# Optimization experiments

Measured on AMD Instinct MI355X. Metric: run time of the kernel, lower is better.

The kernel has to match this reference:

```python
import jax, jax.numpy as jnp
import numpy as np

TAU = 2.0          # spikingjelly LIFNode default
V_TH = 7.0         # from source
DECREASE = 0.5     # decrease_factor
ALPHA = 4.0        # sigmoid surrogate alpha (spikingjelly default)


@jax.custom_vjp
def spike(v):
    # Heaviside with sigmoid surrogate gradient
    return (v >= 0.0).astype(v.dtype)

def _spike_fwd(v):
    return spike(v), v

def _spike_bwd(v, g):
    s = jax.nn.sigmoid(ALPHA * v)
    return (g * ALPHA * s * (1.0 - s),)

spike.defvjp(_spike_fwd, _spike_bwd)


def setup_inputs() -> dict:
    key = jax.random.key(0)
    k1, k2, k3 = jax.random.split(key, 3)
    B, C, T = 4096, 14, 600
    x = jax.random.normal(k1, (B, C, T), dtype=jnp.float32)
    # weights: normal(mean=0.8, std=0.05) clamped to [0,1]; nn.Linear stores [out,in]
    W1 = jnp.clip(0.8 + 0.05 * jax.random.normal(k2, (14, 14), dtype=jnp.float32), 0.0, 1.0)
    W2 = jnp.clip(0.8 + 0.05 * jax.random.normal(k3, (500, 14), dtype=jnp.float32), 0.0, 1.0)
    return {"x": x, "W1": W1, "W2": W2}


def _forward(x, W1, W2):
    B = x.shape[0]
    xt = jnp.transpose(x, (2, 0, 1))  # [T, B, 14]

    v1_0 = jnp.zeros((B, 14), x.dtype)
    v2_0 = jnp.zeros((B, 500), x.dtype)
    cache0 = jnp.zeros((B, 14), x.dtype)

    def step(carry, x_t):
        v1, v2, cache = carry
        # block 1: linear + decayed feedback of previous spikes
        i1 = x_t @ W1.T + DECREASE * cache
        v1 = v1 + (i1 - v1) / TAU          # LIF charge (decay_input, v_reset=0)
        s1 = spike(v1 - V_TH)
        v1 = v1 * (1.0 - s1)               # hard reset to 0
        # block 2
        i2 = s1 @ W2.T
        v2 = v2 + (i2 - v2) / TAU
        s2 = spike(v2 - V_TH)
        v2 = v2 * (1.0 - s2)
        return (v1, v2, s1), None

    (v1, v2, cache), _ = jax.lax.scan(step, (v1_0, v2_0, cache0), xt)
    return jnp.exp(v2)  # liquid state [B, 500]


def reference(x, W1, W2):
    return _forward(x, W1, W2)
```

## Files before the change

### kernel.cpp

```cpp
#include <hip/hip_runtime.h>
#include <math.h>

#define T     600
#define C     14
#define NOUT  500
#define W     128
#define NWIN  5
#define DSTR  132
#define CAP   64

typedef float f32x2 __attribute__((ext_vector_type(2)));

__device__ __forceinline__ void stage16(const float* gp, float* lp) {
    __builtin_amdgcn_global_load_lds(
        (const __attribute__((address_space(1))) void*)(gp),
        (__attribute__((address_space(3))) void*)(lp), 16, 0, 0);
}

__global__ __launch_bounds__(64)
void snn_v8(const float* __restrict__ x, const float* __restrict__ W1,
            const float* __restrict__ W2, float* __restrict__ out) {
    __shared__ float    xs[448 * 4];
    __shared__ float    db[C * DSTR];
    __shared__ unsigned evs[CAP];

    const int  lane = threadIdx.x;
    const long row  = blockIdx.x;
    const float* xr = &x[row * (long)(C * T)];
    const int  ce   = (lane < C) ? lane : (C - 1);

    const float* gsrc[7];
    #pragma unroll
    for (int k = 0; k < 7; ++k) {
        const int s = 64 * k + lane;
        const int j = s >> 5;
        const int g = (s - j) & 31;
        gsrc[k] = xr + j * T + 4 * g;
    }
    int xadr[C];
    #pragma unroll
    for (int j = 0; j < C; ++j)
        xadr[j] = 16 * (32 * j + (((lane >> 1) + j) & 31)) + 8 * (lane & 1);

    #pragma unroll
    for (int k = 0; k < 7; ++k)
        stage16(gsrc[k], &xs[k * 256]);

    float v1 = 0.f;
    int   ecnt = 0;

    for (int w = 0; w < NWIN; ++w) {
        const int t0 = w * W;
        asm volatile("s_waitcnt vmcnt(0)" ::: "memory");
        __builtin_amdgcn_sched_barrier(0);

        f32x2 xv[C];
        #pragma unroll
        for (int j = 0; j < C; ++j)
            xv[j] = *(const f32x2*)((const char*)xs + xadr[j]);
        const float msk = (w == NWIN - 1 && 2 * lane >= T - 512) ? 0.f : 0.5f;
        #pragma unroll
        for (int j = 0; j < C; ++j) { xv[j].x *= msk; xv[j].y *= msk; }
        #pragma unroll
        for (int c = 0; c < C; ++c) {
            f32x2 a = {0.f, 0.f};
            #pragma unroll
            for (int j = 0; j < C; ++j) {
                const float wv = W1[c * C + j];
                a.x = fmaf(xv[j].x, wv, a.x);
                a.y = fmaf(xv[j].y, wv, a.y);
            }
            *(f32x2*)&db[c * DSTR + 2 * lane] = a;
        }
        asm volatile("s_waitcnt lgkmcnt(0)" ::: "memory");
        __builtin_amdgcn_sched_barrier(0);

        if (w + 1 < NWIN) {
            if (w + 1 < NWIN - 1) {
                #pragma unroll
                for (int k = 0; k < 7; ++k) {
                    gsrc[k] += W;
                    stage16(gsrc[k], &xs[k * 256]);
                }
            } else {
                #pragma unroll
                for (int k = 0; k < 7; ++k) {
                    gsrc[k] += W;
                    const int s = 64 * k + lane;
                    const int g = (s - (s >> 5)) & 31;
                    if (4 * g < T - 512)
                        stage16(gsrc[k], &xs[k * 256]);
                }
            }
        }

        const float* dp = &db[ce * DSTR];
        const int nb = (w < NWIN - 1) ? 8 : 6;
        float4 c0 = *(const float4*)&dp[0];
        float4 c1 = *(const float4*)&dp[4];
        float4 c2 = *(const float4*)&dp[8];
        float4 c3 = *(const float4*)&dp[12];
        for (int b = 0; b < nb; ++b) {
            float4 n0, n1, n2, n3;
            const bool more = (b + 1 < nb);
            if (more) {
                const float* np_ = dp + 16 * (b + 1);
                n0 = *(const float4*)&np_[0];
                n1 = *(const float4*)&np_[4];
                n2 = *(const float4*)&np_[8];
                n3 = *(const float4*)&np_[12];
            }
            float h[16];
            h[0]=c0.x; h[1]=c0.y; h[2]=c0.z; h[3]=c0.w;
            h[4]=c1.x; h[5]=c1.y; h[6]=c1.z; h[7]=c1.w;
            h[8]=c2.x; h[9]=c2.y; h[10]=c2.z; h[11]=c2.w;
            h[12]=c3.x; h[13]=c3.y; h[14]=c3.z; h[15]=c3.w;

            float vv = v1;
            float m0 = -1e30f, m1 = -1e30f, m2 = -1e30f, m3 = -1e30f;
            #pragma unroll
            for (int u = 0; u < 16; u += 4) {
                vv = fmaf(vv, 0.5f, h[u]);     m0 = fmaxf(m0, vv);
                vv = fmaf(vv, 0.5f, h[u + 1]); m1 = fmaxf(m1, vv);
                vv = fmaf(vv, 0.5f, h[u + 2]); m2 = fmaxf(m2, vv);
                vv = fmaf(vv, 0.5f, h[u + 3]); m3 = fmaxf(m3, vv);
            }
            const float mx = fmaxf(fmaxf(m0, m1), fmaxf(m2, m3));

            if (__builtin_expect(__ballot(mx >= 7.0f) != 0ull, 0)) {
                float vp = v1;
                #pragma unroll
                for (int u = 0; u < 16; ++u) {
                    vp = fmaf(vp, 0.5f, h[u]);
                    const unsigned long long bal = __ballot(vp >= 7.0f);
                    if (bal) {
                        if (vp >= 7.0f) vp = 0.5f;
                        if (lane == 0 && ecnt < CAP)
                            evs[ecnt] = ((unsigned)(t0 + 16 * b + u) << 14)
                                      | ((unsigned)bal & 0x3FFFu);
                        ++ecnt;
                    }
                }
                v1 = vp;
            } else {
                v1 = vv;
            }
            if (more) { c0 = n0; c1 = n1; c2 = n2; c3 = n3; }
        }
    }

    asm volatile("s_waitcnt lgkmcnt(0)" ::: "memory");
    __builtin_amdgcn_sched_barrier(0);

    const int n = (ecnt < CAP) ? ecnt : CAP;
    float v2[8];
    #pragma unroll
    for (int k = 0; k < 8; ++k) v2[k] = 0.f;
    int tprev = -1;

    for (int e = 0; e < n; ++e) {
        const unsigned ev = evs[e];
        const int t = (int)(ev >> 14);
        unsigned mm = ev & 0x3FFFu;
        float i2[8];
        #pragma unroll
        for (int k = 0; k < 8; ++k) i2[k] = 0.f;
        while (mm) {
            const int c = (int)__builtin_ctz(mm);
            mm &= mm - 1;
            #pragma unroll
            for (int k = 0; k < 8; ++k) {
                const int o = lane + (k << 6);
                if (o < NOUT) i2[k] += W2[o * C + c];
            }
        }
        const int gap = t - tprev - 1;
        if (gap > 0) {
            #pragma unroll
            for (int k = 0; k < 8; ++k) v2[k] = ldexpf(v2[k], -gap);
        }
        #pragma unroll
        for (int k = 0; k < 8; ++k) {
            const float v = v2[k] + (i2[k] - v2[k]) * 0.5f;
            v2[k] = (v >= 7.0f) ? 0.f : v;
        }
        tprev = t;
    }
    {
        const int gap = (T - 1) - tprev;
        if (gap > 0) {
            #pragma unroll
            for (int k = 0; k < 8; ++k) v2[k] = ldexpf(v2[k], -gap);
        }
    }
    #pragma unroll
    for (int k = 0; k < 8; ++k) {
        const int o = lane + (k << 6);
        if (o < NOUT) out[row * NOUT + o] = expf(v2[k]);
    }
}

extern "C" void kernel_launch(void* const* d_in, const int* in_sizes, int n_in,
                              void* d_out, int out_size, void* d_ws, size_t ws_size,
                              hipStream_t stream) {
    const float* x  = (const float*)d_in[0];
    const float* W1 = (const float*)d_in[1];
    const float* W2 = (const float*)d_in[2];
    float* o = (float*)d_out;
    const int B = in_sizes[0] / (C * T);
    snn_v8<<<B, 64, 0, stream>>>(x, W1, W2, o);
}
```

Baseline: 47.81 us.

## Double-buffer x staging in LDS to prefetch two windows ahead

Splits the LDS staging area for input x into two buffers and issues global-to-LDS loads for window w+2 while window w+1's loads are still in flight. It waits with a partial vmcnt(7) instead of a full drain, so global load latency overlaps the recurrent scan over more time. The cost is doubled LDS use for x, which may lower occupancy, plus more complex wait-count bookkeeping that must match the number of outstanding loads.

```diff
diff --git a/kernel.cpp b/kernel.cpp
--- a/kernel.cpp
+++ b/kernel.cpp
@@ -8,6 +8,7 @@
 #define NWIN  5
 #define DSTR  132
 #define CAP   64
+#define XSW   1792
 
 typedef float f32x2 __attribute__((ext_vector_type(2)));
 
@@ -18,9 +19,9 @@
 }
 
 __global__ __launch_bounds__(64)
-void snn_v8(const float* __restrict__ x, const float* __restrict__ W1,
+void snn_v9(const float* __restrict__ x, const float* __restrict__ W1,
             const float* __restrict__ W2, float* __restrict__ out) {
-    __shared__ float    xs[448 * 4];
+    __shared__ float    xs[2 * XSW];
     __shared__ float    db[C * DSTR];
     __shared__ unsigned evs[CAP];
 
@@ -30,12 +31,13 @@
     const int  ce   = (lane < C) ? lane : (C - 1);
 
     const float* gsrc[7];
+    int gk[7];
     #pragma unroll
     for (int k = 0; k < 7; ++k) {
         const int s = 64 * k + lane;
         const int j = s >> 5;
-        const int g = (s - j) & 31;
-        gsrc[k] = xr + j * T + 4 * g;
+        gk[k] = (s - j) & 31;
+        gsrc[k] = xr + j * T + 4 * gk[k];
     }
     int xadr[C];
     #pragma unroll
@@ -43,21 +45,24 @@
         xadr[j] = 16 * (32 * j + (((lane >> 1) + j) & 31)) + 8 * (lane & 1);
 
     #pragma unroll
-    for (int k = 0; k < 7; ++k)
-        stage16(gsrc[k], &xs[k * 256]);
+    for (int k = 0; k < 7; ++k) stage16(gsrc[k],     &xs[k * 256]);
+    #pragma unroll
+    for (int k = 0; k < 7; ++k) stage16(gsrc[k] + W, &xs[XSW + k * 256]);
 
     float v1 = 0.f;
     int   ecnt = 0;
 
     for (int w = 0; w < NWIN; ++w) {
         const int t0 = w * W;
-        asm volatile("s_waitcnt vmcnt(0)" ::: "memory");
+        if (w == NWIN - 1) asm volatile("s_waitcnt vmcnt(0)" ::: "memory");
+        else               asm volatile("s_waitcnt vmcnt(7)" ::: "memory");
         __builtin_amdgcn_sched_barrier(0);
 
+        const char* xb = (const char*)&xs[(w & 1) * XSW];
         f32x2 xv[C];
         #pragma unroll
         for (int j = 0; j < C; ++j)
-            xv[j] = *(const f32x2*)((const char*)xs + xadr[j]);
+            xv[j] = *(const f32x2*)(xb + xadr[j]);
         const float msk = (w == NWIN - 1 && 2 * lane >= T - 512) ? 0.f : 0.5f;
         #pragma unroll
         for (int j = 0; j < C; ++j) { xv[j].x *= msk; xv[j].y *= msk; }
@@ -75,21 +80,20 @@
         asm volatile("s_waitcnt lgkmcnt(0)" ::: "memory");
         __builtin_amdgcn_sched_barrier(0);
 
-        if (w + 1 < NWIN) {
-            if (w + 1 < NWIN - 1) {
+        if (w + 2 < NWIN) {
+            float* lb = &xs[(w & 1) * XSW];
+            if (w + 2 < NWIN - 1) {
                 #pragma unroll
                 for (int k = 0; k < 7; ++k) {
                     gsrc[k] += W;
-                    stage16(gsrc[k], &xs[k * 256]);
+                    stage16(gsrc[k] + W, lb + k * 256);
                 }
             } else {
                 #pragma unroll
                 for (int k = 0; k < 7; ++k) {
                     gsrc[k] += W;
-                    const int s = 64 * k + lane;
-                    const int g = (s - (s >> 5)) & 31;
-                    if (4 * g < T - 512)
-                        stage16(gsrc[k], &xs[k * 256]);
+                    if (4 * gk[k] < T - 512)
+                        stage16(gsrc[k] + W, lb + k * 256);
                 }
             }
         }
@@ -208,5 +212,5 @@
     const float* W2 = (const float*)d_in[2];
     float* o = (float*)d_out;
     const int B = in_sizes[0] / (C * T);
-    snn_v8<<<B, 64, 0, stream>>>(x, W1, W2, o);
+    snn_v9<<<B, 64, 0, stream>>>(x, W1, W2, o);
 }
```

Result: slower. 61.52 us (+28.7%).
